# Optimization experiments

Hardware: AMD Instinct MI355X
Metric: run time of the kernel (lower is better)

The kernel has to match this reference:

```python
import jax, jax.numpy as jnp
import numpy as np

BS, S, D, H, DFF, L = 8, 1024, 256, 8, 1024, 3
DK = D // H
NEG = -1e32


def setup_inputs() -> dict:
    key = jax.random.key(0)
    ks = jax.random.split(key, 10)
    r = lambda k, shp: jax.random.normal(k, shp, jnp.float32) * 0.02
    return {
        "q_embed_data": jax.random.normal(ks[0], (BS, S, D), jnp.float32),
        "qa_embed_data": jax.random.normal(ks[1], (BS, S, D), jnp.float32),
        "Wk": r(ks[2], (L, D, D)), "bk": jnp.zeros((L, D), jnp.float32),
        "Wv": r(ks[3], (L, D, D)), "bv": jnp.zeros((L, D), jnp.float32),
        "Wo": r(ks[4], (L, D, D)), "bo": jnp.zeros((L, D), jnp.float32),
        "gammas": r(ks[5], (L, H)),
        "ln1_g": jnp.ones((L, D), jnp.float32), "ln1_b": jnp.zeros((L, D), jnp.float32),
        "W1": r(ks[6], (L, D, DFF)), "b1": jnp.zeros((L, DFF), jnp.float32),
        "W2": r(ks[7], (L, DFF, D)), "b2": jnp.zeros((L, D), jnp.float32),
        "ln2_g": jnp.ones((L, D), jnp.float32), "ln2_b": jnp.zeros((L, D), jnp.float32),
    }


def _layernorm(x, g, b, eps=1e-5):
    mu = x.mean(-1, keepdims=True)
    var = ((x - mu) ** 2).mean(-1, keepdims=True)
    return (x - mu) * jax.lax.rsqrt(var + eps) * g + b


def _attn(xq, xk, xv, Wk, bk, Wv, bv, Wo, bo, gamma, mask, zero_pad):
    # kq_same=1: q and k both use k_linear
    bs = xq.shape[0]
    q = (xq @ Wk + bk).reshape(bs, S, H, DK).transpose(0, 2, 1, 3)  # bhsd
    k = (xk @ Wk + bk).reshape(bs, S, H, DK).transpose(0, 2, 1, 3)
    v = (xv @ Wv + bv).reshape(bs, S, H, DK).transpose(0, 2, 1, 3)
    scores = jnp.einsum('bhid,bhjd->bhij', q, k) / np.float32(np.sqrt(DK))
    mf = mask.astype(scores.dtype)
    # no-grad decay branch (detached in torch)
    p = jax.nn.softmax(jnp.where(mask, scores, NEG), axis=-1) * mf
    distcum = jnp.cumsum(p, axis=-1)
    disttot = p.sum(axis=-1, keepdims=True)
    idx = jnp.arange(S)
    pos = jnp.abs(idx[None, :] - idx[:, None]).astype(jnp.float32)[None, None]
    dist = jnp.sqrt(jnp.clip((disttot - distcum) * pos, 0.0, None))
    dist = jax.lax.stop_gradient(dist)
    g = -jax.nn.softplus(gamma)[None, :, None, None]  # (1,H,1,1)
    total_effect = jnp.clip(jnp.exp(dist * g), 1e-5, 1e5)
    scores = scores * total_effect
    attn = jax.nn.softmax(jnp.where(mask, scores, NEG), axis=-1)
    if zero_pad:
        attn = attn.at[:, :, 0, :].set(0.0)
    out = jnp.einsum('bhij,bhjd->bhid', attn, v)
    out = out.transpose(0, 2, 1, 3).reshape(bs, S, D)
    return out @ Wo + bo


def _block(i, xq, xk, xv, mask, zero_pad, apply_pos, P):
    Wk, bk, Wv, bv, Wo, bo, gam, l1g, l1b, W1, b1, W2, b2, l2g, l2b = [p[i] for p in P]
    q2 = _attn(xq, xk, xv, Wk, bk, Wv, bv, Wo, bo, gam, mask, zero_pad)
    x = _layernorm(xq + q2, l1g, l1b)
    if apply_pos:
        ff = jax.nn.relu(x @ W1 + b1) @ W2 + b2
        x = _layernorm(x + ff, l2g, l2b)
    return x


def _forward(q_embed_data, qa_embed_data, Wk, bk, Wv, bv, Wo, bo, gammas,
             ln1_g, ln1_b, W1, b1, W2, b2, ln2_g, ln2_b):
    P = (Wk, bk, Wv, bv, Wo, bo, gammas, ln1_g, ln1_b, W1, b1, W2, b2, ln2_g, ln2_b)
    tri_incl = jnp.tril(jnp.ones((S, S), bool))[None, None]       # mask=1: peek current+past
    tri_excl = jnp.tril(jnp.ones((S, S), bool), -1)[None, None]   # mask=0: strictly past
    x, y = q_embed_data, qa_embed_data
    # blocks_1 (n_blocks=1): mask=1, apply_pos=True, self-attn on y
    y = _block(0, y, y, y, tri_incl, False, True, P)
    # blocks_2 (2*n_blocks=2): alternate (mask=1, no FFN) / (mask=0, zero_pad, FFN, values=y)
    x = _block(1, x, x, x, tri_incl, False, False, P)
    x = _block(2, x, x, y, tri_excl, True, True, P)
    return x


def reference(q_embed_data, qa_embed_data, Wk, bk, Wv, bv, Wo, bo, gammas,
              ln1_g, ln1_b, W1, b1, W2, b2, ln2_g, ln2_b):
    return _forward(q_embed_data, qa_embed_data, Wk, bk, Wv, bv, Wo, bo, gammas,
                    ln1_g, ln1_b, W1, b1, W2, b2, ln2_g, ln2_b)
```

## Files before the change

kernel.cpp:

```cpp
#include <hip/hip_runtime.h>

typedef unsigned short u16;
typedef float f32x4 __attribute__((ext_vector_type(4)));
typedef __bf16 bf16x8 __attribute__((ext_vector_type(8)));
typedef u16 u16x8 __attribute__((ext_vector_type(8)));
typedef u16 u16x4 __attribute__((ext_vector_type(4)));

__device__ __forceinline__ u16 f2bf(float f) {
  union { float f; unsigned u; } v; v.f = f;
  unsigned r = (v.u + 0x7FFFu + ((v.u >> 16) & 1u)) >> 16;
  return (u16)r;
}
__device__ __forceinline__ unsigned cvtpk_bf16(float lo, float hi) {
  unsigned r;
  asm("v_cvt_pk_bf16_f32 %0, %1, %2" : "=v"(r) : "v"(lo), "v"(hi));
  return r;
}
__device__ __forceinline__ float wred_sum(float v) {
#pragma unroll
  for (int o = 32; o >= 1; o >>= 1) v += __shfl_xor(v, o);
  return v;
}

template <int RELU, int WF32, int WBF, int WVT>
__global__ __launch_bounds__(256) void gemm_kernel(
    const u16* __restrict__ A, const u16* __restrict__ Bt,
    const float* __restrict__ bias, float* __restrict__ C,
    u16* __restrict__ Cbf, int M, int N, int K) {
  __shared__ u16 As[64 * 64];
  __shared__ u16 Bs[64 * 64];
  const int tid = threadIdx.x;
  const int lane = tid & 63;
  const int w = tid >> 6;
  const int m0 = blockIdx.x * 64;
  const int n0 = blockIdx.y * 64;
  const int wr = (w >> 1) * 32;
  const int wc = (w & 1) * 32;
  const int l15 = lane & 15, hi = lane >> 4;

  f32x4 acc[2][2] = {};

  for (int k0 = 0; k0 < K; k0 += 64) {
#pragma unroll
    for (int rep = 0; rep < 2; ++rep) {
      int idx = tid + rep * 256;
      int row = idx >> 3, c8 = idx & 7;
      int cs = ((c8 ^ (row & 7)) << 3);
      __builtin_amdgcn_global_load_lds(
          (const __attribute__((address_space(1))) void*)(A + (size_t)(m0 + row) * K + k0 + cs),
          (__attribute__((address_space(3))) void*)(&As[idx * 8]), 16, 0, 0);
      __builtin_amdgcn_global_load_lds(
          (const __attribute__((address_space(1))) void*)(Bt + (size_t)(n0 + row) * K + k0 + cs),
          (__attribute__((address_space(3))) void*)(&Bs[idx * 8]), 16, 0, 0);
    }
    __syncthreads();
#pragma unroll
    for (int kk = 0; kk < 2; ++kk) {
      int kb = (kk * 32 + (hi << 3)) << 1;
      bf16x8 af[2], bfr[2];
#pragma unroll
      for (int mf = 0; mf < 2; ++mf) {
        int m = wr + mf * 16 + l15;
        af[mf] = *(const bf16x8*)((const char*)As + m * 128 + (kb ^ ((m & 7) << 4)));
      }
#pragma unroll
      for (int nf = 0; nf < 2; ++nf) {
        int n = wc + nf * 16 + l15;
        bfr[nf] = *(const bf16x8*)((const char*)Bs + n * 128 + (kb ^ ((n & 7) << 4)));
      }
#pragma unroll
      for (int mf = 0; mf < 2; ++mf)
#pragma unroll
        for (int nf = 0; nf < 2; ++nf)
          acc[mf][nf] = __builtin_amdgcn_mfma_f32_16x16x32_bf16(af[mf], bfr[nf], acc[mf][nf], 0, 0, 0);
    }
    __syncthreads();
  }

#pragma unroll
  for (int mf = 0; mf < 2; ++mf)
#pragma unroll
    for (int nf = 0; nf < 2; ++nf) {
      int col = n0 + wc + nf * 16 + l15;
      float bia = bias[col];
      u16x4 tv;
#pragma unroll
      for (int r = 0; r < 4; ++r) {
        int row = m0 + wr + mf * 16 + (hi << 2) + r;
        float val = acc[mf][nf][r] + bia;
        if (RELU) val = fmaxf(val, 0.f);
        if (WF32) C[(size_t)row * N + col] = val;
        if (WBF) Cbf[(size_t)row * N + col] = f2bf(val);
        if (WVT) tv[r] = f2bf(val);
      }
      if (WVT) {
        int row0 = m0 + wr + mf * 16 + (hi << 2);
        size_t addr = (((size_t)(row0 >> 10) * 8 + (col >> 5)) * 32 + (col & 31)) * 1024 + (row0 & 1023);
        *(u16x4*)(Cbf + addr) = tv;
      }
    }
}

__global__ __launch_bounds__(256) void gemm_kv_kernel(
    const u16* __restrict__ A, const u16* __restrict__ Bt,
    const float* __restrict__ biasK, const float* __restrict__ biasV,
    u16* __restrict__ qkbf, u16* __restrict__ vT, int M, int N, int K) {
  __shared__ u16 As[64 * 64];
  __shared__ u16 Bs[64 * 64];
  const int tid = threadIdx.x;
  const int lane = tid & 63;
  const int w = tid >> 6;
  const int m0 = blockIdx.x * 64;
  const int n0 = blockIdx.y * 64;
  const int wr = (w >> 1) * 32;
  const int wc = (w & 1) * 32;
  const int l15 = lane & 15, hi = lane >> 4;

  f32x4 acc[2][2] = {};

  for (int k0 = 0; k0 < K; k0 += 64) {
#pragma unroll
    for (int rep = 0; rep < 2; ++rep) {
      int idx = tid + rep * 256;
      int row = idx >> 3, c8 = idx & 7;
      int cs = ((c8 ^ (row & 7)) << 3);
      __builtin_amdgcn_global_load_lds(
          (const __attribute__((address_space(1))) void*)(A + (size_t)(m0 + row) * K + k0 + cs),
          (__attribute__((address_space(3))) void*)(&As[idx * 8]), 16, 0, 0);
      __builtin_amdgcn_global_load_lds(
          (const __attribute__((address_space(1))) void*)(Bt + (size_t)(n0 + row) * K + k0 + cs),
          (__attribute__((address_space(3))) void*)(&Bs[idx * 8]), 16, 0, 0);
    }
    __syncthreads();
#pragma unroll
    for (int kk = 0; kk < 2; ++kk) {
      int kb = (kk * 32 + (hi << 3)) << 1;
      bf16x8 af[2], bfr[2];
#pragma unroll
      for (int mf = 0; mf < 2; ++mf) {
        int m = wr + mf * 16 + l15;
        af[mf] = *(const bf16x8*)((const char*)As + m * 128 + (kb ^ ((m & 7) << 4)));
      }
#pragma unroll
      for (int nf = 0; nf < 2; ++nf) {
        int n = wc + nf * 16 + l15;
        bfr[nf] = *(const bf16x8*)((const char*)Bs + n * 128 + (kb ^ ((n & 7) << 4)));
      }
#pragma unroll
      for (int mf = 0; mf < 2; ++mf)
#pragma unroll
        for (int nf = 0; nf < 2; ++nf)
          acc[mf][nf] = __builtin_amdgcn_mfma_f32_16x16x32_bf16(af[mf], bfr[nf], acc[mf][nf], 0, 0, 0);
    }
    __syncthreads();
  }

  const bool isV = (n0 >= 256);
#pragma unroll
  for (int mf = 0; mf < 2; ++mf)
#pragma unroll
    for (int nf = 0; nf < 2; ++nf) {
      int col = n0 + wc + nf * 16 + l15;
      float bia = isV ? biasV[col - 256] : biasK[col];
      u16x4 tv;
#pragma unroll
      for (int r = 0; r < 4; ++r) {
        int row = m0 + wr + mf * 16 + (hi << 2) + r;
        float val = acc[mf][nf][r] + bia;
        if (!isV) qkbf[(size_t)row * 256 + col] = f2bf(val);
        tv[r] = f2bf(val);
      }
      if (isV) {
        int row0 = m0 + wr + mf * 16 + (hi << 2);
        int vc = col - 256;
        size_t addr = (((size_t)(row0 >> 10) * 8 + (vc >> 5)) * 32 + (vc & 31)) * 1024 + (row0 & 1023);
        *(u16x4*)(vT + addr) = tv;
      }
    }
}

__global__ __launch_bounds__(256) void attn_mfma_kernel(
    const u16* __restrict__ qkbf, const u16* __restrict__ vT,
    u16* __restrict__ ao, const float* __restrict__ gam, int excl) {
  __shared__ float zbuf[4][16];
  __shared__ float z2buf[4][16];
  __shared__ float accbuf[8][4][64];

  const int lane = threadIdx.x & 63, w = threadIdx.x >> 6;
  const int qt = 63 - blockIdx.y;
  const int bh = blockIdx.x;
  const int b = bh >> 3, h = bh & 7;
  const int q0 = qt * 16;
  const int l15 = lane & 15, hi = lane >> 4;
  const int i = q0 + l15;
  const float g = -log1pf(__expf(gam[h]));
  const float scale = 0.17677669529663687f;

  const u16* kbase = qkbf + ((size_t)b * 1024) * 256 + h * 32;
  const bf16x8 qfrag = *(const bf16x8*)(kbase + (size_t)i * 256 + hi * 8);

  const int mylim = i - excl;
  const int jmax = q0 + 15 - excl;
  const int ntiles = (jmax >> 4) + 1;
  const int C = (ntiles + 3) >> 2;
  const int c0 = w * C;
  const int tEnd = (c0 + C < ntiles) ? (c0 + C) : ntiles;
  const int count = (tEnd > c0) ? (tEnd - c0) : 0;

  float zacc = 0.f;
  for (int t = c0; t < tEnd; ++t) {
    bf16x8 kf = *(const bf16x8*)(kbase + (size_t)(t * 16 + l15) * 256 + hi * 8);
    f32x4 sA = {};
    sA = __builtin_amdgcn_mfma_f32_16x16x32_bf16(kf, qfrag, sA, 0, 0, 0);
    if (t == ntiles - 1) {
      const int kb = t * 16 + hi * 4;
#pragma unroll
      for (int r = 0; r < 4; ++r)
        zacc += (kb + r <= mylim) ? __expf(sA[r] * scale) : 0.f;
    } else {
#pragma unroll
      for (int r = 0; r < 4; ++r) zacc += __expf(sA[r] * scale);
    }
  }
  zacc += __shfl_xor(zacc, 16);
  zacc += __shfl_xor(zacc, 32);
  if (lane < 16) zbuf[w][lane] = zacc;
  __syncthreads();

  const float zc0 = zbuf[0][l15], zc1 = zbuf[1][l15];
  const float zc2 = zbuf[2][l15], zc3 = zbuf[3][l15];
  const float Z = zc0 + zc1 + zc2 + zc3;
  const float invZ = Z > 0.f ? 1.f / Z : 0.f;
  float prefix = 0.f;
  if (w > 0) prefix += zc0;
  if (w > 1) prefix += zc1;
  if (w > 2) prefix += zc2;

  const u16* vbase = vT + (size_t)bh * 32 * 1024;
  float carry = prefix, z2 = 0.f;
  f32x4 accO0 = {}, accO1 = {};
  unsigned pk00 = 0, pk01 = 0;
  const int Cp = (count + 1) & ~1;

  f32x4 sA_cur = {};
  if (count > 0) {
    bf16x8 kf = *(const bf16x8*)(kbase + (size_t)(c0 * 16 + l15) * 256 + hi * 8);
    sA_cur = __builtin_amdgcn_mfma_f32_16x16x32_bf16(kf, qfrag, sA_cur, 0, 0, 0);
  }
  for (int tl = 0; tl < Cp; ++tl) {
    const int t = c0 + tl;
    f32x4 sA_nxt = {};
    if (tl + 1 < count) {
      bf16x8 kf = *(const bf16x8*)(kbase + (size_t)((t + 1) * 16 + l15) * 256 + hi * 8);
      sA_nxt = __builtin_amdgcn_mfma_f32_16x16x32_bf16(kf, qfrag, sA_nxt, 0, 0, 0);
    }
    float ep0 = 0.f, ep1 = 0.f, ep2 = 0.f, ep3 = 0.f;
    if (tl < count) {
      const int kb = t * 16 + hi * 4;
      const bool diag = (t == ntiles - 1);
      const float sv0 = sA_cur[0] * scale, sv1 = sA_cur[1] * scale;
      const float sv2 = sA_cur[2] * scale, sv3 = sA_cur[3] * scale;
      float e0 = __expf(sv0), e1 = __expf(sv1);
      float e2 = __expf(sv2), e3 = __expf(sv3);
      bool m0 = true, m1 = true, m2 = true, m3 = true;
      if (diag) {
        m0 = (kb + 0 <= mylim); m1 = (kb + 1 <= mylim);
        m2 = (kb + 2 <= mylim); m3 = (kb + 3 <= mylim);
        e0 = m0 ? e0 : 0.f; e1 = m1 ? e1 : 0.f;
        e2 = m2 ? e2 : 0.f; e3 = m3 ? e3 : 0.f;
      }
      const float cA = e0 + e1, cB = cA + e2, cC = cB + e3;
      float vsc = cC;
      float tmp = __shfl_up(vsc, 16); if (hi >= 1) vsc += tmp;
      tmp = __shfl_up(vsc, 32); if (hi >= 2) vsc += tmp;
      const float exg = vsc - cC;
      const float tot = __shfl(vsc, l15 + 48);
      const float cb = carry + exg;
      carry += tot;
      const float posb = (float)(i - kb);
      const float cum0 = cb + e0, cum1 = cb + cA, cum2 = cb + cB, cum3 = cb + cC;
      const float d20 = fmaxf((Z - cum0) * invZ * posb, 0.f);
      const float d21 = fmaxf((Z - cum1) * invZ * (posb - 1.f), 0.f);
      const float d22 = fmaxf((Z - cum2) * invZ * (posb - 2.f), 0.f);
      const float d23 = fmaxf((Z - cum3) * invZ * (posb - 3.f), 0.f);
      const float te0 = fmaxf(__expf(__builtin_amdgcn_sqrtf(d20) * g), 1e-5f);
      const float te1 = fmaxf(__expf(__builtin_amdgcn_sqrtf(d21) * g), 1e-5f);
      const float te2 = fmaxf(__expf(__builtin_amdgcn_sqrtf(d22) * g), 1e-5f);
      const float te3 = fmaxf(__expf(__builtin_amdgcn_sqrtf(d23) * g), 1e-5f);
      ep0 = __expf(sv0 * te0); ep1 = __expf(sv1 * te1);
      ep2 = __expf(sv2 * te2); ep3 = __expf(sv3 * te3);
      if (diag) {
        ep0 = m0 ? ep0 : 0.f; ep1 = m1 ? ep1 : 0.f;
        ep2 = m2 ? ep2 : 0.f; ep3 = m3 ? ep3 : 0.f;
      }
      z2 += (ep0 + ep1) + (ep2 + ep3);
    }
    const unsigned u0 = cvtpk_bf16(ep0, ep1);
    const unsigned u1 = cvtpk_bf16(ep2, ep3);
    if ((tl & 1) == 0) {
      pk00 = u0; pk01 = u1;
    } else {
      const int srcA = l15 + (((2 * hi) & 3) << 4);
      const int srcB = l15 + (((2 * hi + 1) & 3) << 4);
      unsigned a00 = (unsigned)__shfl((int)pk00, srcA);
      unsigned a01 = (unsigned)__shfl((int)u0,   srcA);
      unsigned a10 = (unsigned)__shfl((int)pk01, srcA);
      unsigned a11 = (unsigned)__shfl((int)u1,   srcA);
      unsigned b00 = (unsigned)__shfl((int)pk00, srcB);
      unsigned b01 = (unsigned)__shfl((int)u0,   srcB);
      unsigned b10 = (unsigned)__shfl((int)pk01, srcB);
      unsigned b11 = (unsigned)__shfl((int)u1,   srcB);
      const bool up = hi >= 2;
      union { unsigned u[4]; bf16x8 v; } pf;
      pf.u[0] = up ? a01 : a00;
      pf.u[1] = up ? a11 : a10;
      pf.u[2] = up ? b01 : b00;
      pf.u[3] = up ? b11 : b10;
      const int jb = (t - 1) * 16;
      bf16x8 vf0 = *(const bf16x8*)(vbase + (size_t)l15 * 1024 + jb + hi * 8);
      bf16x8 vf1 = *(const bf16x8*)(vbase + (size_t)(16 + l15) * 1024 + jb + hi * 8);
      accO0 = __builtin_amdgcn_mfma_f32_16x16x32_bf16(vf0, pf.v, accO0, 0, 0, 0);
      accO1 = __builtin_amdgcn_mfma_f32_16x16x32_bf16(vf1, pf.v, accO1, 0, 0, 0);
    }
    sA_cur = sA_nxt;
  }

  z2 += __shfl_xor(z2, 16);
  z2 += __shfl_xor(z2, 32);
  if (lane < 16) z2buf[w][lane] = z2;
#pragma unroll
  for (int j = 0; j < 4; ++j) {
    accbuf[j][w][lane] = accO0[j];
    accbuf[4 + j][w][lane] = accO1[j];
  }
  __syncthreads();

  if (w == 0) {
    const float z2t = z2buf[0][l15] + z2buf[1][l15] + z2buf[2][l15] + z2buf[3][l15];
    const float inv2 = z2t > 0.f ? 1.f / z2t : 0.f;
    u16* aop = ao + ((size_t)(b * 1024 + i)) * 256 + h * 32;
    float s0[4], s1[4];
#pragma unroll
    for (int j = 0; j < 4; ++j) {
      s0[j] = (accbuf[j][0][lane] + accbuf[j][1][lane] + accbuf[j][2][lane] + accbuf[j][3][lane]) * inv2;
      s1[j] = (accbuf[4 + j][0][lane] + accbuf[4 + j][1][lane] + accbuf[4 + j][2][lane] + accbuf[4 + j][3][lane]) * inv2;
    }
    uint2 o0, o1;
    o0.x = cvtpk_bf16(s0[0], s0[1]); o0.y = cvtpk_bf16(s0[2], s0[3]);
    o1.x = cvtpk_bf16(s1[0], s1[1]); o1.y = cvtpk_bf16(s1[2], s1[3]);
    *(uint2*)(aop + hi * 4) = o0;
    *(uint2*)(aop + 16 + hi * 4) = o1;
  }
}

__global__ __launch_bounds__(256) void add_ln_kernel(
    const float* __restrict__ res, const float* __restrict__ add,
    const float* __restrict__ g, const float* __restrict__ b,
    float* __restrict__ outf, u16* __restrict__ outb) {
  const int lane = threadIdx.x & 63, wid = threadIdx.x >> 6;
  const size_t row = (size_t)blockIdx.x * 4 + wid;
  const size_t base = row * 256 + lane * 4;
  float4 rv = *(const float4*)(res + base);
  float4 av = *(const float4*)(add + base);
  float x0 = rv.x + av.x, x1 = rv.y + av.y, x2 = rv.z + av.z, x3 = rv.w + av.w;
  float sm = wred_sum(x0 + x1 + x2 + x3);
  float mu = sm * (1.f / 256.f);
  float d0 = x0 - mu, d1 = x1 - mu, d2 = x2 - mu, d3 = x3 - mu;
  float vs = wred_sum(d0 * d0 + d1 * d1 + d2 * d2 + d3 * d3);
  float rs = rsqrtf(vs * (1.f / 256.f) + 1e-5f);
  float4 gv = *(const float4*)(g + lane * 4);
  float4 bv = *(const float4*)(b + lane * 4);
  float o0 = d0 * rs * gv.x + bv.x;
  float o1 = d1 * rs * gv.y + bv.y;
  float o2 = d2 * rs * gv.z + bv.z;
  float o3 = d3 * rs * gv.w + bv.w;
  float4 ov = {o0, o1, o2, o3};
  *(float4*)(outf + base) = ov;
  u16x4 wv; wv[0] = f2bf(o0); wv[1] = f2bf(o1); wv[2] = f2bf(o2); wv[3] = f2bf(o3);
  *(u16x4*)(outb + base) = wv;
}

__global__ __launch_bounds__(256) void cast_bf_kernel(
    const float* __restrict__ in, u16* __restrict__ out) {
  size_t i = ((size_t)blockIdx.x * 256 + threadIdx.x) * 8;
  float4 a = *(const float4*)(in + i);
  float4 c = *(const float4*)(in + i + 4);
  u16x8 o;
  o[0] = f2bf(a.x); o[1] = f2bf(a.y); o[2] = f2bf(a.z); o[3] = f2bf(a.w);
  o[4] = f2bf(c.x); o[5] = f2bf(c.y); o[6] = f2bf(c.z); o[7] = f2bf(c.w);
  *(u16x8*)(out + i) = o;
}

__global__ __launch_bounds__(256) void transpose_cast_kernel(
    const float* __restrict__ W, u16* __restrict__ Wt, int K, int N,
    int dstStride) {
  __shared__ float t[32][33];
  const size_t lo = (size_t)blockIdx.z * K * N;
  const size_t lod = (size_t)blockIdx.z * dstStride;
  int n0 = blockIdx.x * 32, k0 = blockIdx.y * 32;
  int tx = threadIdx.x, ty = threadIdx.y;
#pragma unroll
  for (int r = 0; r < 32; r += 8)
    t[ty + r][tx] = W[lo + (size_t)(k0 + ty + r) * N + n0 + tx];
  __syncthreads();
#pragma unroll
  for (int r = 0; r < 32; r += 8)
    Wt[lod + (size_t)(n0 + ty + r) * K + k0 + tx] = f2bf(t[tx][ty + r]);
}

extern "C" void kernel_launch(void* const* d_in, const int* in_sizes, int n_in,
                              void* d_out, int out_size, void* d_ws,
                              size_t ws_size, hipStream_t stream) {
  const float* q_embed = (const float*)d_in[0];
  const float* qa_embed = (const float*)d_in[1];
  const float* Wk = (const float*)d_in[2];
  const float* bk = (const float*)d_in[3];
  const float* Wv = (const float*)d_in[4];
  const float* bv = (const float*)d_in[5];
  const float* Wo = (const float*)d_in[6];
  const float* bo = (const float*)d_in[7];
  const float* gammas = (const float*)d_in[8];
  const float* ln1_g = (const float*)d_in[9];
  const float* ln1_b = (const float*)d_in[10];
  const float* W1 = (const float*)d_in[11];
  const float* b1 = (const float*)d_in[12];
  const float* W2 = (const float*)d_in[13];
  const float* b2 = (const float*)d_in[14];
  const float* ln2_g = (const float*)d_in[15];
  const float* ln2_b = (const float*)d_in[16];

  const size_t ACT_F32 = (size_t)8192 * 256 * 4;
  const size_t ACT_BF = (size_t)8192 * 256 * 2;
  char* p = (char*)d_ws;
  auto carve = [&](size_t bytes) {
    void* r = (void*)p;
    p += (bytes + 255) & ~(size_t)255;
    return r;
  };
  float* yb = (float*)carve(ACT_F32);
  float* xb = (float*)carve(ACT_F32);
  float* pof = (float*)carve(ACT_F32);
  u16* xbf = (u16*)carve(ACT_BF);
  u16* ybf = (u16*)carve(ACT_BF);
  u16* qkbf = (u16*)carve(ACT_BF);
  u16* vTb = (u16*)carve(ACT_BF);
  u16* aobf = (u16*)carve(ACT_BF);
  u16* hbf = (u16*)carve((size_t)8192 * 1024 * 2);
  u16* Wkvt = (u16*)carve((size_t)3 * 131072 * 2);
  u16* Wot = (u16*)carve((size_t)3 * 65536 * 2);
  u16* W1t = (u16*)carve((size_t)3 * 262144 * 2);
  u16* W2t = (u16*)carve((size_t)3 * 262144 * 2);

  dim3 tb(32, 8);
  transpose_cast_kernel<<<dim3(8, 8, 3), tb, 0, stream>>>(Wk, Wkvt, 256, 256, 131072);
  transpose_cast_kernel<<<dim3(8, 8, 3), tb, 0, stream>>>(Wv, Wkvt + 65536, 256, 256, 131072);
  transpose_cast_kernel<<<dim3(8, 8, 3), tb, 0, stream>>>(Wo, Wot, 256, 256, 65536);
  transpose_cast_kernel<<<dim3(32, 8, 3), tb, 0, stream>>>(W1, W1t, 256, 1024, 262144);
  transpose_cast_kernel<<<dim3(8, 32, 3), tb, 0, stream>>>(W2, W2t, 1024, 256, 262144);
  cast_bf_kernel<<<1024, 256, 0, stream>>>(q_embed, xbf);
  cast_bf_kernel<<<1024, 256, 0, stream>>>(qa_embed, ybf);

  const dim3 gP(128, 4), gF(128, 16), gKV(128, 8);
  const dim3 gA(64, 64);

  gemm_kv_kernel<<<gKV, 256, 0, stream>>>(ybf, Wkvt, bk, bv, qkbf, vTb, 8192, 512, 256);
  attn_mfma_kernel<<<gA, 256, 0, stream>>>(qkbf, vTb, aobf, gammas, 0);
  gemm_kernel<0, 1, 0, 0><<<gP, 256, 0, stream>>>(aobf, Wot, bo, pof, nullptr, 8192, 256, 256);
  add_ln_kernel<<<2048, 256, 0, stream>>>(qa_embed, pof, ln1_g, ln1_b, yb, ybf);
  gemm_kernel<1, 0, 1, 0><<<gF, 256, 0, stream>>>(ybf, W1t, b1, nullptr, hbf, 8192, 1024, 256);
  gemm_kernel<0, 1, 0, 0><<<gP, 256, 0, stream>>>(hbf, W2t, b2, pof, nullptr, 8192, 256, 1024);
  add_ln_kernel<<<2048, 256, 0, stream>>>(yb, pof, ln2_g, ln2_b, yb, ybf);

  gemm_kv_kernel<<<gKV, 256, 0, stream>>>(xbf, Wkvt + 131072, bk + 256, bv + 256, qkbf, vTb, 8192, 512, 256);
  attn_mfma_kernel<<<gA, 256, 0, stream>>>(qkbf, vTb, aobf, gammas + 8, 0);
  gemm_kernel<0, 1, 0, 0><<<gP, 256, 0, stream>>>(aobf, Wot + 65536, bo + 256, pof, nullptr, 8192, 256, 256);
  add_ln_kernel<<<2048, 256, 0, stream>>>(q_embed, pof, ln1_g + 256, ln1_b + 256, xb, xbf);

  gemm_kv_kernel<<<gKV, 256, 0, stream>>>(xbf, Wkvt + 262144, bk + 512, bv + 512, qkbf, vTb, 8192, 512, 256);
  gemm_kernel<0, 0, 0, 1><<<gP, 256, 0, stream>>>(ybf, Wkvt + 262144 + 65536, bv + 512, nullptr, vTb, 8192, 256, 256);
  attn_mfma_kernel<<<gA, 256, 0, stream>>>(qkbf, vTb, aobf, gammas + 16, 1);
  gemm_kernel<0, 1, 0, 0><<<gP, 256, 0, stream>>>(aobf, Wot + 131072, bo + 512, pof, nullptr, 8192, 256, 256);
  add_ln_kernel<<<2048, 256, 0, stream>>>(xb, pof, ln1_g + 512, ln1_b + 512, xb, xbf);
  gemm_kernel<1, 0, 1, 0><<<gF, 256, 0, stream>>>(xbf, W1t + 524288, b1 + 2048, nullptr, hbf, 8192, 1024, 256);
  gemm_kernel<0, 1, 0, 0><<<gP, 256, 0, stream>>>(hbf, W2t + 524288, b2 + 512, pof, nullptr, 8192, 256, 1024);
  add_ln_kernel<<<2048, 256, 0, stream>>>(xb, pof, ln2_g + 512, ln2_b + 512, (float*)d_out, xbf);
}
```

Baseline: 305.2 us.

## Cache attention logits in fp16 registers instead of recomputing QK scores

The first pass now keeps the scaled logits for each key tile in a register array of packed fp16 values, and the second pass reads them back instead of reissuing the K loads and QK MFMAs. All exponentials switch to exp2 with log2e folded into the scale, the decay factor and the clip. The second loop is fully unrolled over a fixed maximum of 16 tiles with the two-tile pairing made explicit. This removes the duplicate global K reads and matrix ops, but adds register pressure (32 extra VGPRs), fp16 rounding of the logits, and assumes each wave never handles more than 16 tiles.

```diff
diff --git a/kernel.cpp b/kernel.cpp
--- a/kernel.cpp
+++ b/kernel.cpp
@@ -5,6 +5,7 @@
 typedef __bf16 bf16x8 __attribute__((ext_vector_type(8)));
 typedef u16 u16x8 __attribute__((ext_vector_type(8)));
 typedef u16 u16x4 __attribute__((ext_vector_type(4)));
+typedef __fp16 h16x2 __attribute__((ext_vector_type(2)));
 
 __device__ __forceinline__ u16 f2bf(float f) {
   union { float f; unsigned u; } v; v.f = f;
@@ -15,6 +16,15 @@
   unsigned r;
   asm("v_cvt_pk_bf16_f32 %0, %1, %2" : "=v"(r) : "v"(lo), "v"(hi));
   return r;
+}
+__device__ __forceinline__ unsigned pk_f16(float a, float b) {
+  union { h16x2 h; unsigned u; } v;
+  v.h = __builtin_amdgcn_cvt_pkrtz(a, b);
+  return v.u;
+}
+__device__ __forceinline__ float2 unpk_f16(unsigned u) {
+  union { unsigned u; h16x2 h; } v; v.u = u;
+  return make_float2((float)v.h.x, (float)v.h.y);
 }
 __device__ __forceinline__ float wred_sum(float v) {
 #pragma unroll
@@ -193,8 +203,10 @@
   const int q0 = qt * 16;
   const int l15 = lane & 15, hi = lane >> 4;
   const int i = q0 + l15;
-  const float g = -log1pf(__expf(gam[h]));
-  const float scale = 0.17677669529663687f;
+  const float LOG2E = 1.4426950408889634f;
+  const float g2 = -log1pf(__expf(gam[h])) * LOG2E;
+  const float cscale = 0.17677669529663687f * LOG2E;
+  const float CLIP2 = -16.609640474436812f;
 
   const u16* kbase = qkbf + ((size_t)b * 1024) * 256 + h * 32;
   const bf16x8 qfrag = *(const bf16x8*)(kbase + (size_t)i * 256 + hi * 8);
@@ -207,19 +219,30 @@
   const int tEnd = (c0 + C < ntiles) ? (c0 + C) : ntiles;
   const int count = (tEnd > c0) ? (tEnd - c0) : 0;
 
+  unsigned lpk[32];
   float zacc = 0.f;
-  for (int t = c0; t < tEnd; ++t) {
-    bf16x8 kf = *(const bf16x8*)(kbase + (size_t)(t * 16 + l15) * 256 + hi * 8);
-    f32x4 sA = {};
-    sA = __builtin_amdgcn_mfma_f32_16x16x32_bf16(kf, qfrag, sA, 0, 0, 0);
-    if (t == ntiles - 1) {
-      const int kb = t * 16 + hi * 4;
-#pragma unroll
-      for (int r = 0; r < 4; ++r)
-        zacc += (kb + r <= mylim) ? __expf(sA[r] * scale) : 0.f;
+#pragma unroll
+  for (int tl = 0; tl < 16; ++tl) {
+    if (tl < count) {
+      const int t = c0 + tl;
+      bf16x8 kf = *(const bf16x8*)(kbase + (size_t)(t * 16 + l15) * 256 + hi * 8);
+      f32x4 sA = {};
+      sA = __builtin_amdgcn_mfma_f32_16x16x32_bf16(kf, qfrag, sA, 0, 0, 0);
+      float l0 = sA[0] * cscale, l1 = sA[1] * cscale;
+      float l2 = sA[2] * cscale, l3 = sA[3] * cscale;
+      if (t == ntiles - 1) {
+        const int kb = t * 16 + hi * 4;
+        l0 = (kb + 0 <= mylim) ? l0 : -1000.f;
+        l1 = (kb + 1 <= mylim) ? l1 : -1000.f;
+        l2 = (kb + 2 <= mylim) ? l2 : -1000.f;
+        l3 = (kb + 3 <= mylim) ? l3 : -1000.f;
+      }
+      zacc += (exp2f(l0) + exp2f(l1)) + (exp2f(l2) + exp2f(l3));
+      lpk[2 * tl] = pk_f16(l0, l1);
+      lpk[2 * tl + 1] = pk_f16(l2, l3);
     } else {
-#pragma unroll
-      for (int r = 0; r < 4; ++r) zacc += __expf(sA[r] * scale);
+      lpk[2 * tl] = 0xE3D0E3D0u;
+      lpk[2 * tl + 1] = 0xE3D0E3D0u;
     }
   }
   zacc += __shfl_xor(zacc, 16);
@@ -239,67 +262,51 @@
   const u16* vbase = vT + (size_t)bh * 32 * 1024;
   float carry = prefix, z2 = 0.f;
   f32x4 accO0 = {}, accO1 = {};
-  unsigned pk00 = 0, pk01 = 0;
   const int Cp = (count + 1) & ~1;
 
-  f32x4 sA_cur = {};
-  if (count > 0) {
-    bf16x8 kf = *(const bf16x8*)(kbase + (size_t)(c0 * 16 + l15) * 256 + hi * 8);
-    sA_cur = __builtin_amdgcn_mfma_f32_16x16x32_bf16(kf, qfrag, sA_cur, 0, 0, 0);
-  }
-  for (int tl = 0; tl < Cp; ++tl) {
-    const int t = c0 + tl;
-    f32x4 sA_nxt = {};
-    if (tl + 1 < count) {
-      bf16x8 kf = *(const bf16x8*)(kbase + (size_t)((t + 1) * 16 + l15) * 256 + hi * 8);
-      sA_nxt = __builtin_amdgcn_mfma_f32_16x16x32_bf16(kf, qfrag, sA_nxt, 0, 0, 0);
-    }
-    float ep0 = 0.f, ep1 = 0.f, ep2 = 0.f, ep3 = 0.f;
-    if (tl < count) {
-      const int kb = t * 16 + hi * 4;
-      const bool diag = (t == ntiles - 1);
-      const float sv0 = sA_cur[0] * scale, sv1 = sA_cur[1] * scale;
-      const float sv2 = sA_cur[2] * scale, sv3 = sA_cur[3] * scale;
-      float e0 = __expf(sv0), e1 = __expf(sv1);
-      float e2 = __expf(sv2), e3 = __expf(sv3);
-      bool m0 = true, m1 = true, m2 = true, m3 = true;
-      if (diag) {
-        m0 = (kb + 0 <= mylim); m1 = (kb + 1 <= mylim);
-        m2 = (kb + 2 <= mylim); m3 = (kb + 3 <= mylim);
-        e0 = m0 ? e0 : 0.f; e1 = m1 ? e1 : 0.f;
-        e2 = m2 ? e2 : 0.f; e3 = m3 ? e3 : 0.f;
-      }
-      const float cA = e0 + e1, cB = cA + e2, cC = cB + e3;
-      float vsc = cC;
-      float tmp = __shfl_up(vsc, 16); if (hi >= 1) vsc += tmp;
-      tmp = __shfl_up(vsc, 32); if (hi >= 2) vsc += tmp;
-      const float exg = vsc - cC;
-      const float tot = __shfl(vsc, l15 + 48);
-      const float cb = carry + exg;
-      carry += tot;
-      const float posb = (float)(i - kb);
-      const float cum0 = cb + e0, cum1 = cb + cA, cum2 = cb + cB, cum3 = cb + cC;
-      const float d20 = fmaxf((Z - cum0) * invZ * posb, 0.f);
-      const float d21 = fmaxf((Z - cum1) * invZ * (posb - 1.f), 0.f);
-      const float d22 = fmaxf((Z - cum2) * invZ * (posb - 2.f), 0.f);
-      const float d23 = fmaxf((Z - cum3) * invZ * (posb - 3.f), 0.f);
-      const float te0 = fmaxf(__expf(__builtin_amdgcn_sqrtf(d20) * g), 1e-5f);
-      const float te1 = fmaxf(__expf(__builtin_amdgcn_sqrtf(d21) * g), 1e-5f);
-      const float te2 = fmaxf(__expf(__builtin_amdgcn_sqrtf(d22) * g), 1e-5f);
-      const float te3 = fmaxf(__expf(__builtin_amdgcn_sqrtf(d23) * g), 1e-5f);
-      ep0 = __expf(sv0 * te0); ep1 = __expf(sv1 * te1);
-      ep2 = __expf(sv2 * te2); ep3 = __expf(sv3 * te3);
-      if (diag) {
-        ep0 = m0 ? ep0 : 0.f; ep1 = m1 ? ep1 : 0.f;
-        ep2 = m2 ? ep2 : 0.f; ep3 = m3 ? ep3 : 0.f;
-      }
-      z2 += (ep0 + ep1) + (ep2 + ep3);
-    }
-    const unsigned u0 = cvtpk_bf16(ep0, ep1);
-    const unsigned u1 = cvtpk_bf16(ep2, ep3);
-    if ((tl & 1) == 0) {
-      pk00 = u0; pk01 = u1;
-    } else {
+  auto tile_sm = [&](int tlocal, unsigned pa, unsigned pb,
+                     unsigned& u0, unsigned& u1) {
+    float2 v01 = unpk_f16(pa), v23 = unpk_f16(pb);
+    const float l0 = v01.x, l1 = v01.y, l2 = v23.x, l3 = v23.y;
+    const float e0 = exp2f(l0), e1 = exp2f(l1);
+    const float e2 = exp2f(l2), e3 = exp2f(l3);
+    const float cA = e0 + e1, cB = cA + e2, cC = cB + e3;
+    float vsc = cC;
+    float tmp = __shfl_up(vsc, 16); if (hi >= 1) vsc += tmp;
+    tmp = __shfl_up(vsc, 32); if (hi >= 2) vsc += tmp;
+    const float exg = vsc - cC;
+    const float tot = __shfl(vsc, l15 + 48);
+    const float cb = carry + exg;
+    carry += tot;
+    const int kb = (c0 + tlocal) * 16 + hi * 4;
+    const float posb = (float)(i - kb);
+    const float r0 = (Z - (cb + e0)) * invZ;
+    const float r1 = (Z - (cb + cA)) * invZ;
+    const float r2 = (Z - (cb + cB)) * invZ;
+    const float r3 = (Z - (cb + cC)) * invZ;
+    const float d20 = fmaxf(r0 * posb, 0.f);
+    const float d21 = fmaxf(r1 * (posb - 1.f), 0.f);
+    const float d22 = fmaxf(r2 * (posb - 2.f), 0.f);
+    const float d23 = fmaxf(r3 * (posb - 3.f), 0.f);
+    const float a0 = fmaxf(__builtin_amdgcn_sqrtf(d20) * g2, CLIP2);
+    const float a1 = fmaxf(__builtin_amdgcn_sqrtf(d21) * g2, CLIP2);
+    const float a2 = fmaxf(__builtin_amdgcn_sqrtf(d22) * g2, CLIP2);
+    const float a3 = fmaxf(__builtin_amdgcn_sqrtf(d23) * g2, CLIP2);
+    const float p0 = exp2f(l0 * exp2f(a0));
+    const float p1 = exp2f(l1 * exp2f(a1));
+    const float p2 = exp2f(l2 * exp2f(a2));
+    const float p3 = exp2f(l3 * exp2f(a3));
+    z2 += (p0 + p1) + (p2 + p3);
+    u0 = cvtpk_bf16(p0, p1);
+    u1 = cvtpk_bf16(p2, p3);
+  };
+
+#pragma unroll
+  for (int pp = 0; pp < 8; ++pp) {
+    if (2 * pp < Cp) {
+      unsigned pk00, pk01, u0, u1;
+      tile_sm(2 * pp, lpk[4 * pp], lpk[4 * pp + 1], pk00, pk01);
+      tile_sm(2 * pp + 1, lpk[4 * pp + 2], lpk[4 * pp + 3], u0, u1);
       const int srcA = l15 + (((2 * hi) & 3) << 4);
       const int srcB = l15 + (((2 * hi + 1) & 3) << 4);
       unsigned a00 = (unsigned)__shfl((int)pk00, srcA);
@@ -316,13 +323,12 @@
       pf.u[1] = up ? a11 : a10;
       pf.u[2] = up ? b01 : b00;
       pf.u[3] = up ? b11 : b10;
-      const int jb = (t - 1) * 16;
+      const int jb = (c0 + 2 * pp) * 16;
       bf16x8 vf0 = *(const bf16x8*)(vbase + (size_t)l15 * 1024 + jb + hi * 8);
       bf16x8 vf1 = *(const bf16x8*)(vbase + (size_t)(16 + l15) * 1024 + jb + hi * 8);
       accO0 = __builtin_amdgcn_mfma_f32_16x16x32_bf16(vf0, pf.v, accO0, 0, 0, 0);
       accO1 = __builtin_amdgcn_mfma_f32_16x16x32_bf16(vf1, pf.v, accO1, 0, 0, 0);
     }
-    sA_cur = sA_nxt;
   }
 
   z2 += __shfl_xor(z2, 16);
```

Measured after the change: 298.3 us. 1.02x faster.
